# Performance work log

Measured on AMD Instinct MI355X. Metric: run time of the kernel, lower is better.

Reference implementation:

```python
import jax, jax.numpy as jnp
import numpy as np


def fps_single(xyz, npoint):
    """Furthest point sampling. xyz: [N,3] -> [npoint] int32 indices (first = 0)."""
    d0 = jnp.sum((xyz - xyz[0]) ** 2, axis=-1)  # [N]

    def body(dists, _):
        nxt = jnp.argmax(dists)
        d = jnp.sum((xyz - xyz[nxt]) ** 2, axis=-1)
        return jnp.minimum(dists, d), nxt.astype(jnp.int32)

    _, idxs = jax.lax.scan(body, d0, None, length=npoint - 1)
    return jnp.concatenate([jnp.zeros((1,), jnp.int32), idxs])


def setup_inputs() -> dict:
    key = jax.random.key(0)
    k1, k2 = jax.random.split(key)
    B, N, C = 4, 8192, 128
    points = jax.random.normal(k1, (B, N, 3), dtype=jnp.float32)
    features = jax.random.normal(k2, (B, C, N), dtype=jnp.float32)
    return {"points": points, "features": features, "npoint": 2048, "nsample": 16}


def reference(points, features, npoint, nsample):
    """FPS downsample -> kNN grouping (mean pool) -> three_nn inverse-distance interpolation.
    points: [B,N,3], features: [B,C,N]. Returns interpolated features [B,C,N]."""
    B, N, _ = points.shape
    # --- furthest point sampling (Sample module) ---
    fps_idx = jax.vmap(lambda p: fps_single(p, npoint))(points)          # [B,Q]
    xyz_q = jnp.take_along_axis(points, fps_idx[..., None], axis=1)      # [B,Q,3]
    # --- pairwise squared distances query->all (pdist2squared) ---
    sq = (jnp.sum(xyz_q ** 2, -1)[:, :, None]
          + jnp.sum(points ** 2, -1)[:, None, :]
          - 2.0 * jnp.einsum('bqd,bnd->bqn', xyz_q, points))             # [B,Q,N]
    sq = jnp.maximum(sq, 0.0)
    # --- kNN neighbors, drop self (SampleNeighbors, knn=True takes topk nsample+1 then [:,:,1:]) ---
    _, nbr = jax.lax.top_k(-sq, nsample + 1)                             # [B,Q,K+1]
    nbr = nbr[..., 1:]                                                   # [B,Q,K]
    grouped = jax.vmap(lambda f, idx: f[:, idx])(features, nbr)          # [B,C,Q,K]
    coarse = jnp.mean(grouped, axis=-1)                                  # [B,C,Q]
    # --- three_nn + inverse squared-distance interpolation (GraphFPModule) ---
    neg_d3, i3 = jax.lax.top_k(-jnp.swapaxes(sq, 1, 2), 3)               # [B,N,3]
    d3 = jnp.maximum(-neg_d3, 1e-10)                                     # squared dists, clamped
    inv = 1.0 / (d3 + 1e-8)
    w = inv / jnp.sum(inv, axis=-1, keepdims=True)                       # [B,N,3]
    f3 = jax.vmap(lambda f, idx: f[:, idx])(coarse, i3)                  # [B,C,N,3]
    out = jnp.sum(f3 * w[:, None, :, :], axis=-1)                        # [B,C,N]
    return out
```

## Files before the change

kernel.cpp:

```cpp
#include <hip/hip_runtime.h>
#include <cstdint>
#include <cstddef>

#define Bq   4
#define Nq   8192
#define Cq   128
#define NPq  2048
#define NSq  16
#define KSEL 17

__device__ __forceinline__ float rn_sq3(float x, float y, float z) {
  return __fadd_rn(__fadd_rn(__fmul_rn(x, x), __fmul_rn(y, y)), __fmul_rn(z, z));
}

__device__ __forceinline__ float sq_expand(float qx, float qy, float qz, float sq_,
                                           float px, float py, float pz, float sp_) {
  float dot = __fadd_rn(__fadd_rn(__fmul_rn(qx, px), __fmul_rn(qy, py)), __fmul_rn(qz, pz));
  float v = __fsub_rn(__fadd_rn(sq_, sp_), __fmul_rn(2.0f, dot));
  v = fmaxf(v, 0.0f);
  return __fadd_rn(v, 0.0f);
}

__global__ __launch_bounds__(256) void k_sump(const float* __restrict__ pts,
                                              float* __restrict__ sump) {
  int g = blockIdx.x * 256 + threadIdx.x;
  float x = pts[g * 3 + 0], y = pts[g * 3 + 1], z = pts[g * 3 + 2];
  sump[g] = rn_sq3(x, y, z);
}

__global__ __launch_bounds__(512) void k_fps(const float* __restrict__ pts,
                                             int* __restrict__ fps_idx) {
  const int b = blockIdx.x;
  const int tid = threadIdx.x;
  const int lane = tid & 63, wid = tid >> 6;
  const float* P = pts + (size_t)b * Nq * 3;

  __shared__ unsigned long long wkeys[2][8];

  float px[16], py[16], pz[16], dd[16];
#pragma unroll
  for (int k = 0; k < 16; k++) {
    int p = k * 512 + tid;
    px[k] = P[p * 3 + 0];
    py[k] = P[p * 3 + 1];
    pz[k] = P[p * 3 + 2];
  }
  float qx = P[0], qy = P[1], qz = P[2];
  float bd = -1.0f;
  int bk = 0;
#pragma unroll
  for (int k = 0; k < 16; k++) {
    float d = rn_sq3(__fsub_rn(px[k], qx), __fsub_rn(py[k], qy), __fsub_rn(pz[k], qz));
    dd[k] = d;
    if (d > bd) { bd = d; bk = k; }
  }
  int bp = (bk << 9) + tid;
  if (tid == 0) fps_idx[b * NPq] = 0;

  for (int i = 1; i < NPq; i++) {
    unsigned long long key =
        ((unsigned long long)__float_as_uint(bd) << 32) | (unsigned int)(~(unsigned int)bp);
#pragma unroll
    for (int off = 32; off > 0; off >>= 1) {
      unsigned long long o = __shfl_down(key, off);
      key = o > key ? o : key;
    }
    if (lane == 0) wkeys[i & 1][wid] = key;
    __syncthreads();

    unsigned long long m = wkeys[i & 1][0];
#pragma unroll
    for (int w = 1; w < 8; w++) {
      unsigned long long t = wkeys[i & 1][w];
      m = t > m ? t : m;
    }
    unsigned int p = ~(unsigned int)m;
    if (tid == 0) fps_idx[b * NPq + i] = (int)p;

    const float* cp = P + 3u * p;
    float cx = cp[0], cy = cp[1], cz = cp[2];

    bd = -1.0f;
    bk = 0;
#pragma unroll
    for (int k = 0; k < 16; k++) {
      float d = rn_sq3(__fsub_rn(px[k], cx), __fsub_rn(py[k], cy), __fsub_rn(pz[k], cz));
      float nd = fminf(dd[k], d);
      dd[k] = nd;
      if (nd > bd) { bd = nd; bk = k; }
    }
    bp = (bk << 9) + tid;
  }
}

__global__ __launch_bounds__(256) void k_gatherq(const float* __restrict__ pts,
                                                 const float* __restrict__ sump,
                                                 const int* __restrict__ fps_idx,
                                                 float* __restrict__ xyzq,
                                                 float* __restrict__ sumq) {
  int g = blockIdx.x * 256 + threadIdx.x;
  int b = g >> 11;
  int idx = fps_idx[g];
  int src = b * Nq + idx;
  xyzq[g * 3 + 0] = pts[src * 3 + 0];
  xyzq[g * 3 + 1] = pts[src * 3 + 1];
  xyzq[g * 3 + 2] = pts[src * 3 + 2];
  sumq[g] = sump[src];
}

__global__ __launch_bounds__(256) void k_knn_group(const float* __restrict__ pts,
                                                   const float* __restrict__ sump,
                                                   const float* __restrict__ xyzq,
                                                   const float* __restrict__ sumq,
                                                   const float* __restrict__ feats,
                                                   float* __restrict__ coarse_t) {
  const int blk = blockIdx.x;
  const int b = blk >> 11;
  const int tid = threadIdx.x;
  const int lane = tid & 63, wid = tid >> 6;
  const float* P = pts + (size_t)b * Nq * 3;
  const float* SP = sump + (size_t)b * Nq;

  __shared__ float sq_lds[Nq];
  __shared__ unsigned long long wkeys[4];
  __shared__ int sel[KSEL];

  float qx = xyzq[blk * 3 + 0], qy = xyzq[blk * 3 + 1], qz = xyzq[blk * 3 + 2];
  float sq_ = sumq[blk];

#pragma unroll
  for (int k = 0; k < 32; k++) {
    int p = k * 256 + tid;
    float x = P[p * 3 + 0], y = P[p * 3 + 1], z = P[p * 3 + 2];
    sq_lds[p] = sq_expand(qx, qy, qz, sq_, x, y, z, SP[p]);
  }
  __syncthreads();

  for (int r = 0; r < KSEL; r++) {
    unsigned long long best = ~0ull;
#pragma unroll
    for (int k = 0; k < 32; k++) {
      int p = k * 256 + tid;
      unsigned long long key =
          ((unsigned long long)__float_as_uint(sq_lds[p]) << 32) | (unsigned int)p;
      best = key < best ? key : best;
    }
#pragma unroll
    for (int off = 32; off > 0; off >>= 1) {
      unsigned long long o = __shfl_down(best, off);
      best = o < best ? o : best;
    }
    if (lane == 0) wkeys[wid] = best;
    __syncthreads();
    if (tid == 0) {
      unsigned long long m = wkeys[0];
      m = wkeys[1] < m ? wkeys[1] : m;
      m = wkeys[2] < m ? wkeys[2] : m;
      m = wkeys[3] < m ? wkeys[3] : m;
      int p = (int)(unsigned int)(m & 0xFFFFFFFFull);
      sel[r] = p;
      sq_lds[p] = __uint_as_float(0x7f800000u);
    }
    __syncthreads();
  }

  if (tid < Cq) {
    const float* F = feats + ((size_t)(b * Cq + tid)) * Nq;
    float acc = 0.0f;
#pragma unroll
    for (int j = 1; j < KSEL; j++) acc += F[sel[j]];
    coarse_t[(size_t)blk * Cq + tid] = acc * (1.0f / 16.0f);
  }
}

__device__ __forceinline__ void merge3(unsigned long long& a0, unsigned long long& a1,
                                       unsigned long long& a2, unsigned long long b0,
                                       unsigned long long b1, unsigned long long b2) {
  unsigned long long lo1 = a0 < b0 ? a0 : b0;
  unsigned long long hi1 = a0 < b0 ? b0 : a0;
  unsigned long long lo2 = a1 < b1 ? a1 : b1;
  unsigned long long hi2 = a1 < b1 ? b1 : a1;
  unsigned long long lo3 = a2 < b2 ? a2 : b2;
  unsigned long long c1 = hi1 < lo2 ? hi1 : lo2;
  unsigned long long m1 = hi1 < lo2 ? lo2 : hi1;
  unsigned long long m2 = hi2 < lo3 ? hi2 : lo3;
  a0 = lo1;
  a1 = c1;
  a2 = m1 < m2 ? m1 : m2;
}

__global__ __launch_bounds__(256) void k_three(const float* __restrict__ pts,
                                               const float* __restrict__ sump,
                                               const float* __restrict__ xyzq,
                                               const float* __restrict__ sumq,
                                               int* __restrict__ i0, int* __restrict__ i1,
                                               int* __restrict__ i2, float* __restrict__ w0,
                                               float* __restrict__ w1, float* __restrict__ w2) {
  const int wid = threadIdx.x >> 6, lane = threadIdx.x & 63;
  const int n = blockIdx.x * 4 + wid;
  const int b = n >> 13;
  float px = pts[n * 3 + 0], py = pts[n * 3 + 1], pz = pts[n * 3 + 2];
  float sp = sump[n];
  const float* XQ = xyzq + (size_t)b * NPq * 3;
  const float* SQ = sumq + (size_t)b * NPq;

  unsigned long long k0 = ~0ull, k1 = ~0ull, k2 = ~0ull;
#pragma unroll 4
  for (int j = 0; j < 32; j++) {
    int q = lane + j * 64;
    float v = sq_expand(XQ[q * 3 + 0], XQ[q * 3 + 1], XQ[q * 3 + 2], SQ[q], px, py, pz, sp);
    unsigned long long key = ((unsigned long long)__float_as_uint(v) << 32) | (unsigned int)q;
    if (key < k2) {
      if (key < k1) {
        k2 = k1;
        if (key < k0) { k1 = k0; k0 = key; } else { k1 = key; }
      } else {
        k2 = key;
      }
    }
  }
#pragma unroll
  for (int off = 32; off > 0; off >>= 1) {
    unsigned long long o0 = __shfl_down(k0, off);
    unsigned long long o1 = __shfl_down(k1, off);
    unsigned long long o2 = __shfl_down(k2, off);
    merge3(k0, k1, k2, o0, o1, o2);
  }
  if (lane == 0) {
    float v0 = __uint_as_float((unsigned int)(k0 >> 32));
    float v1 = __uint_as_float((unsigned int)(k1 >> 32));
    float v2 = __uint_as_float((unsigned int)(k2 >> 32));
    float d0 = fmaxf(v0, 1e-10f), d1 = fmaxf(v1, 1e-10f), d2 = fmaxf(v2, 1e-10f);
    float inv0 = 1.0f / (d0 + 1e-8f);
    float inv1 = 1.0f / (d1 + 1e-8f);
    float inv2 = 1.0f / (d2 + 1e-8f);
    float s = inv0 + inv1 + inv2;
    i0[n] = (int)(unsigned int)(k0 & 0xFFFFFFFFull);
    i1[n] = (int)(unsigned int)(k1 & 0xFFFFFFFFull);
    i2[n] = (int)(unsigned int)(k2 & 0xFFFFFFFFull);
    w0[n] = inv0 / s;
    w1[n] = inv1 / s;
    w2[n] = inv2 / s;
  }
}

__global__ __launch_bounds__(256) void k_interp(const float* __restrict__ coarse_t,
                                                const int* __restrict__ i0,
                                                const int* __restrict__ i1,
                                                const int* __restrict__ i2,
                                                const float* __restrict__ w0,
                                                const float* __restrict__ w1,
                                                const float* __restrict__ w2,
                                                float* __restrict__ out) {
  int g = blockIdx.x * 256 + threadIdx.x;
  int b = g >> 13, n = g & (Nq - 1);
  int a0 = i0[g], a1 = i1[g], a2 = i2[g];
  float u0 = w0[g], u1 = w1[g], u2 = w2[g];
  const float4* r0 = (const float4*)(coarse_t + ((size_t)b * NPq + a0) * Cq);
  const float4* r1 = (const float4*)(coarse_t + ((size_t)b * NPq + a1) * Cq);
  const float4* r2 = (const float4*)(coarse_t + ((size_t)b * NPq + a2) * Cq);
  float* O = out + (size_t)b * Cq * Nq + n;
#pragma unroll 4
  for (int cq = 0; cq < Cq / 4; cq++) {
    float4 f0 = r0[cq], f1 = r1[cq], f2 = r2[cq];
    float o0 = u0 * f0.x + u1 * f1.x + u2 * f2.x;
    float o1 = u0 * f0.y + u1 * f1.y + u2 * f2.y;
    float o2 = u0 * f0.z + u1 * f1.z + u2 * f2.z;
    float o3 = u0 * f0.w + u1 * f1.w + u2 * f2.w;
    O[(size_t)(cq * 4 + 0) * Nq] = o0;
    O[(size_t)(cq * 4 + 1) * Nq] = o1;
    O[(size_t)(cq * 4 + 2) * Nq] = o2;
    O[(size_t)(cq * 4 + 3) * Nq] = o3;
  }
}

extern "C" void kernel_launch(void* const* d_in, const int* in_sizes, int n_in,
                              void* d_out, int out_size, void* d_ws, size_t ws_size,
                              hipStream_t stream) {
  const float* pts = (const float*)d_in[0];
  const float* feats = (const float*)d_in[1];
  float* out = (float*)d_out;

  char* ws = (char*)d_ws;
  size_t off = 0;
  auto alloc = [&](size_t bytes) {
    void* p = ws + off;
    off += (bytes + 255) & ~(size_t)255;
    return p;
  };
  float* sump = (float*)alloc((size_t)Bq * Nq * 4);
  int* fps_idx = (int*)alloc((size_t)Bq * NPq * 4);
  float* xyzq = (float*)alloc((size_t)Bq * NPq * 3 * 4);
  float* sumq = (float*)alloc((size_t)Bq * NPq * 4);
  float* coarse_t = (float*)alloc((size_t)Bq * NPq * Cq * 4);
  int* i0 = (int*)alloc((size_t)Bq * Nq * 4);
  int* i1 = (int*)alloc((size_t)Bq * Nq * 4);
  int* i2 = (int*)alloc((size_t)Bq * Nq * 4);
  float* w0 = (float*)alloc((size_t)Bq * Nq * 4);
  float* w1 = (float*)alloc((size_t)Bq * Nq * 4);
  float* w2 = (float*)alloc((size_t)Bq * Nq * 4);

  k_sump<<<(Bq * Nq) / 256, 256, 0, stream>>>(pts, sump);
  k_fps<<<Bq, 512, 0, stream>>>(pts, fps_idx);
  k_gatherq<<<(Bq * NPq) / 256, 256, 0, stream>>>(pts, sump, fps_idx, xyzq, sumq);
  k_knn_group<<<Bq * NPq, 256, 0, stream>>>(pts, sump, xyzq, sumq, feats, coarse_t);
  k_three<<<(Bq * Nq) / 4, 256, 0, stream>>>(pts, sump, xyzq, sumq, i0, i1, i2, w0, w1, w2);
  k_interp<<<(Bq * Nq) / 256, 256, 0, stream>>>(coarse_t, i0, i1, i2, w0, w1, w2, out);
}
```

Before: 2.770 ms.

## Speed up FPS reduction with DPP, incremental kNN selection, SoA query layout

Several changes land together. FPS now uses packed 2-wide float math with contiguous per-thread points. Its per-wave argmax becomes a DPP float max plus a ballot, which replaces the 64-bit shuffle reduction. kNN selection keeps a per-thread running minimum and rescans only in the thread that owned the removed point, which removes one barrier per round and avoids full rescans. k_three reads query coordinates from new SoA arrays so loads coalesce. The changes risk tie-breaking differences: the ballot picks the lowest lane rather than the lowest index, and the contiguous point assignment changes which index wins on ties.

Result: faster. 2.412 ms (-12.9%).

```diff
diff --git a/kernel.cpp b/kernel.cpp
--- a/kernel.cpp
+++ b/kernel.cpp
@@ -6,11 +6,21 @@
 #define Nq   8192
 #define Cq   128
 #define NPq  2048
-#define NSq  16
 #define KSEL 17
+
+typedef float v2f __attribute__((ext_vector_type(2)));
 
 __device__ __forceinline__ float rn_sq3(float x, float y, float z) {
   return __fadd_rn(__fadd_rn(__fmul_rn(x, x), __fmul_rn(y, y)), __fmul_rn(z, z));
+}
+
+__device__ __forceinline__ v2f dist2_v2(v2f px, v2f py, v2f pz, float cx, float cy, float cz) {
+#pragma clang fp contract(off)
+  v2f dx = px - cx;
+  v2f dy = py - cy;
+  v2f dz = pz - cz;
+  v2f s = dx * dx + dy * dy + dz * dz;
+  return s;
 }
 
 __device__ __forceinline__ float sq_expand(float qx, float qy, float qz, float sq_,
@@ -28,6 +38,12 @@
   sump[g] = rn_sq3(x, y, z);
 }
 
+template <int CTRL, int RM, int BM>
+__device__ __forceinline__ float dpp_maxf(float v) {
+  int r = __builtin_amdgcn_update_dpp(__float_as_int(v), __float_as_int(v), CTRL, RM, BM, false);
+  return fmaxf(v, __int_as_float(r));
+}
+
 __global__ __launch_bounds__(512) void k_fps(const float* __restrict__ pts,
                                              int* __restrict__ fps_idx) {
   const int b = blockIdx.x;
@@ -35,61 +51,74 @@
   const int lane = tid & 63, wid = tid >> 6;
   const float* P = pts + (size_t)b * Nq * 3;
 
-  __shared__ unsigned long long wkeys[2][8];
-
-  float px[16], py[16], pz[16], dd[16];
-#pragma unroll
-  for (int k = 0; k < 16; k++) {
-    int p = k * 512 + tid;
-    px[k] = P[p * 3 + 0];
-    py[k] = P[p * 3 + 1];
-    pz[k] = P[p * 3 + 2];
+  __shared__ float sv[2][8];
+  __shared__ int spi[2][8];
+
+  v2f px[8], py[8], pz[8], dd[8];
+  const int pbase = tid * 16;
+#pragma unroll
+  for (int j = 0; j < 8; j++) {
+    const float2* q2 = (const float2*)(P + (size_t)(pbase + 2 * j) * 3);
+    float2 A = q2[0], Bv = q2[1], Cv = q2[2];
+    v2f tx, ty, tz;
+    tx.x = A.x;  tx.y = Bv.y;
+    ty.x = A.y;  ty.y = Cv.x;
+    tz.x = Bv.x; tz.y = Cv.y;
+    px[j] = tx; py[j] = ty; pz[j] = tz;
   }
   float qx = P[0], qy = P[1], qz = P[2];
   float bd = -1.0f;
-  int bk = 0;
-#pragma unroll
-  for (int k = 0; k < 16; k++) {
-    float d = rn_sq3(__fsub_rn(px[k], qx), __fsub_rn(py[k], qy), __fsub_rn(pz[k], qz));
-    dd[k] = d;
-    if (d > bd) { bd = d; bk = k; }
-  }
-  int bp = (bk << 9) + tid;
+  int bp = pbase;
+#pragma unroll
+  for (int j = 0; j < 8; j++) {
+    v2f s = dist2_v2(px[j], py[j], pz[j], qx, qy, qz);
+    dd[j] = s;
+    if (s.x > bd) { bd = s.x; bp = pbase + 2 * j; }
+    if (s.y > bd) { bd = s.y; bp = pbase + 2 * j + 1; }
+  }
   if (tid == 0) fps_idx[b * NPq] = 0;
 
   for (int i = 1; i < NPq; i++) {
-    unsigned long long key =
-        ((unsigned long long)__float_as_uint(bd) << 32) | (unsigned int)(~(unsigned int)bp);
-#pragma unroll
-    for (int off = 32; off > 0; off >>= 1) {
-      unsigned long long o = __shfl_down(key, off);
-      key = o > key ? o : key;
-    }
-    if (lane == 0) wkeys[i & 1][wid] = key;
+    float wv = bd;
+    wv = dpp_maxf<0x111, 0xf, 0xf>(wv);
+    wv = dpp_maxf<0x112, 0xf, 0xf>(wv);
+    wv = dpp_maxf<0x114, 0xf, 0xf>(wv);
+    wv = dpp_maxf<0x118, 0xf, 0xf>(wv);
+    wv = dpp_maxf<0x142, 0xa, 0xf>(wv);
+    wv = dpp_maxf<0x143, 0xc, 0xf>(wv);
+    float wmax = __int_as_float(__builtin_amdgcn_readlane(__float_as_int(wv), 63));
+    unsigned long long msk = __ballot(bd == wmax);
+    int wl = (int)__ffsll(msk) - 1;
+    int wbp = __shfl(bp, wl);
+    if (lane == 0) { sv[i & 1][wid] = wmax; spi[i & 1][wid] = wbp; }
     __syncthreads();
 
-    unsigned long long m = wkeys[i & 1][0];
+    float bv = sv[i & 1][0];
+    int bip = spi[i & 1][0];
 #pragma unroll
     for (int w = 1; w < 8; w++) {
-      unsigned long long t = wkeys[i & 1][w];
-      m = t > m ? t : m;
-    }
-    unsigned int p = ~(unsigned int)m;
-    if (tid == 0) fps_idx[b * NPq + i] = (int)p;
-
-    const float* cp = P + 3u * p;
+      float tv = sv[i & 1][w];
+      bool t = tv > bv;
+      bv = t ? tv : bv;
+      bip = t ? spi[i & 1][w] : bip;
+    }
+    if (tid == 0) fps_idx[b * NPq + i] = bip;
+
+    const float* cp = P + (size_t)bip * 3;
     float cx = cp[0], cy = cp[1], cz = cp[2];
 
     bd = -1.0f;
-    bk = 0;
-#pragma unroll
-    for (int k = 0; k < 16; k++) {
-      float d = rn_sq3(__fsub_rn(px[k], cx), __fsub_rn(py[k], cy), __fsub_rn(pz[k], cz));
-      float nd = fminf(dd[k], d);
-      dd[k] = nd;
-      if (nd > bd) { bd = nd; bk = k; }
-    }
-    bp = (bk << 9) + tid;
+    bp = pbase;
+#pragma unroll
+    for (int j = 0; j < 8; j++) {
+      v2f s = dist2_v2(px[j], py[j], pz[j], cx, cy, cz);
+      v2f nd;
+      nd.x = fminf(dd[j].x, s.x);
+      nd.y = fminf(dd[j].y, s.y);
+      dd[j] = nd;
+      if (nd.x > bd) { bd = nd.x; bp = pbase + 2 * j; }
+      if (nd.y > bd) { bd = nd.y; bp = pbase + 2 * j + 1; }
+    }
   }
 }
 
@@ -97,14 +126,19 @@
                                                  const float* __restrict__ sump,
                                                  const int* __restrict__ fps_idx,
                                                  float* __restrict__ xyzq,
-                                                 float* __restrict__ sumq) {
+                                                 float* __restrict__ sumq,
+                                                 float* __restrict__ xqs,
+                                                 float* __restrict__ yqs,
+                                                 float* __restrict__ zqs) {
   int g = blockIdx.x * 256 + threadIdx.x;
   int b = g >> 11;
   int idx = fps_idx[g];
   int src = b * Nq + idx;
-  xyzq[g * 3 + 0] = pts[src * 3 + 0];
-  xyzq[g * 3 + 1] = pts[src * 3 + 1];
-  xyzq[g * 3 + 2] = pts[src * 3 + 2];
+  float x = pts[src * 3 + 0], y = pts[src * 3 + 1], z = pts[src * 3 + 2];
+  xyzq[g * 3 + 0] = x;
+  xyzq[g * 3 + 1] = y;
+  xyzq[g * 3 + 2] = z;
+  xqs[g] = x; yqs[g] = y; zqs[g] = z;
   sumq[g] = sump[src];
 }
 
@@ -122,47 +156,51 @@
   const float* SP = sump + (size_t)b * Nq;
 
   __shared__ float sq_lds[Nq];
-  __shared__ unsigned long long wkeys[4];
+  __shared__ unsigned long long wk[2][4];
   __shared__ int sel[KSEL];
 
   float qx = xyzq[blk * 3 + 0], qy = xyzq[blk * 3 + 1], qz = xyzq[blk * 3 + 2];
   float sq_ = sumq[blk];
 
+  unsigned long long lmin = ~0ull;
 #pragma unroll
   for (int k = 0; k < 32; k++) {
     int p = k * 256 + tid;
     float x = P[p * 3 + 0], y = P[p * 3 + 1], z = P[p * 3 + 2];
-    sq_lds[p] = sq_expand(qx, qy, qz, sq_, x, y, z, SP[p]);
+    float v = sq_expand(qx, qy, qz, sq_, x, y, z, SP[p]);
+    sq_lds[p] = v;
+    unsigned long long key = ((unsigned long long)__float_as_uint(v) << 32) | (unsigned int)p;
+    lmin = key < lmin ? key : lmin;
+  }
+
+  for (int r = 0; r < KSEL; r++) {
+    unsigned long long key = lmin;
+#pragma unroll
+    for (int off = 32; off > 0; off >>= 1) {
+      unsigned long long o = __shfl_down(key, off);
+      key = o < key ? o : key;
+    }
+    if (lane == 0) wk[r & 1][wid] = key;
+    __syncthreads();
+    unsigned long long m = wk[r & 1][0];
+    m = wk[r & 1][1] < m ? wk[r & 1][1] : m;
+    m = wk[r & 1][2] < m ? wk[r & 1][2] : m;
+    m = wk[r & 1][3] < m ? wk[r & 1][3] : m;
+    int p = (int)(unsigned int)(m & 0xFFFFFFFFull);
+    if (tid == 0) sel[r] = p;
+    if ((p & 255) == tid) {
+      sq_lds[p] = __uint_as_float(0x7f800000u);
+      lmin = ~0ull;
+#pragma unroll
+      for (int k = 0; k < 32; k++) {
+        int pp = k * 256 + tid;
+        unsigned long long kk =
+            ((unsigned long long)__float_as_uint(sq_lds[pp]) << 32) | (unsigned int)pp;
+        lmin = kk < lmin ? kk : lmin;
+      }
+    }
   }
   __syncthreads();
-
-  for (int r = 0; r < KSEL; r++) {
-    unsigned long long best = ~0ull;
-#pragma unroll
-    for (int k = 0; k < 32; k++) {
-      int p = k * 256 + tid;
-      unsigned long long key =
-          ((unsigned long long)__float_as_uint(sq_lds[p]) << 32) | (unsigned int)p;
-      best = key < best ? key : best;
-    }
-#pragma unroll
-    for (int off = 32; off > 0; off >>= 1) {
-      unsigned long long o = __shfl_down(best, off);
-      best = o < best ? o : best;
-    }
-    if (lane == 0) wkeys[wid] = best;
-    __syncthreads();
-    if (tid == 0) {
-      unsigned long long m = wkeys[0];
-      m = wkeys[1] < m ? wkeys[1] : m;
-      m = wkeys[2] < m ? wkeys[2] : m;
-      m = wkeys[3] < m ? wkeys[3] : m;
-      int p = (int)(unsigned int)(m & 0xFFFFFFFFull);
-      sel[r] = p;
-      sq_lds[p] = __uint_as_float(0x7f800000u);
-    }
-    __syncthreads();
-  }
 
   if (tid < Cq) {
     const float* F = feats + ((size_t)(b * Cq + tid)) * Nq;
@@ -191,7 +229,9 @@
 
 __global__ __launch_bounds__(256) void k_three(const float* __restrict__ pts,
                                                const float* __restrict__ sump,
-                                               const float* __restrict__ xyzq,
+                                               const float* __restrict__ xqs,
+                                               const float* __restrict__ yqs,
+                                               const float* __restrict__ zqs,
                                                const float* __restrict__ sumq,
                                                int* __restrict__ i0, int* __restrict__ i1,
                                                int* __restrict__ i2, float* __restrict__ w0,
@@ -201,14 +241,16 @@
   const int b = n >> 13;
   float px = pts[n * 3 + 0], py = pts[n * 3 + 1], pz = pts[n * 3 + 2];
   float sp = sump[n];
-  const float* XQ = xyzq + (size_t)b * NPq * 3;
+  const float* QX = xqs + (size_t)b * NPq;
+  const float* QY = yqs + (size_t)b * NPq;
+  const float* QZ = zqs + (size_t)b * NPq;
   const float* SQ = sumq + (size_t)b * NPq;
 
   unsigned long long k0 = ~0ull, k1 = ~0ull, k2 = ~0ull;
 #pragma unroll 4
   for (int j = 0; j < 32; j++) {
     int q = lane + j * 64;
-    float v = sq_expand(XQ[q * 3 + 0], XQ[q * 3 + 1], XQ[q * 3 + 2], SQ[q], px, py, pz, sp);
+    float v = sq_expand(QX[q], QY[q], QZ[q], SQ[q], px, py, pz, sp);
     unsigned long long key = ((unsigned long long)__float_as_uint(v) << 32) | (unsigned int)q;
     if (key < k2) {
       if (key < k1) {
@@ -299,11 +341,14 @@
   float* w0 = (float*)alloc((size_t)Bq * Nq * 4);
   float* w1 = (float*)alloc((size_t)Bq * Nq * 4);
   float* w2 = (float*)alloc((size_t)Bq * Nq * 4);
+  float* xqs = (float*)alloc((size_t)Bq * NPq * 4);
+  float* yqs = (float*)alloc((size_t)Bq * NPq * 4);
+  float* zqs = (float*)alloc((size_t)Bq * NPq * 4);
 
   k_sump<<<(Bq * Nq) / 256, 256, 0, stream>>>(pts, sump);
   k_fps<<<Bq, 512, 0, stream>>>(pts, fps_idx);
-  k_gatherq<<<(Bq * NPq) / 256, 256, 0, stream>>>(pts, sump, fps_idx, xyzq, sumq);
+  k_gatherq<<<(Bq * NPq) / 256, 256, 0, stream>>>(pts, sump, fps_idx, xyzq, sumq, xqs, yqs, zqs);
   k_knn_group<<<Bq * NPq, 256, 0, stream>>>(pts, sump, xyzq, sumq, feats, coarse_t);
-  k_three<<<(Bq * Nq) / 4, 256, 0, stream>>>(pts, sump, xyzq, sumq, i0, i1, i2, w0, w1, w2);
+  k_three<<<(Bq * Nq) / 4, 256, 0, stream>>>(pts, sump, xqs, yqs, zqs, sumq, i0, i1, i2, w0, w1, w2);
   k_interp<<<(Bq * Nq) / 256, 256, 0, stream>>>(coarse_t, i0, i1, i2, w0, w1, w2, out);
 }
```
